# Performance work log

Hardware: AMD Instinct MI355X
Metric: run time of the kernel (lower is better)

Reference implementation:

```python
import jax, jax.numpy as jnp
import numpy as np

N_NODES = 16384
N_GRAPHS = 64
NODES_PER_GRAPH = N_NODES // N_GRAPHS
F_IN = 128
E_DIM = 256
N_HEADS = 8
MLP = 1024
N_LAYERS = 4
N_CLASSES = 10
N_EDGES = 262144
LN_EPS = 1e-5


def setup_inputs() -> dict:
    key = jax.random.key(0)
    ks = jax.random.split(key, 32)
    s = 0.02
    inp = {
        "x": jax.random.normal(ks[0], (N_NODES, F_IN), jnp.float32),
        "edge_idx": jax.random.randint(ks[1], (2, N_EDGES), 0, N_NODES, jnp.int32),
        "batch": (jnp.arange(N_NODES, dtype=jnp.int32) // NODES_PER_GRAPH),
        "pos_enc": jax.random.normal(ks[2], (N_NODES, E_DIM), jnp.float32),
        # GCNConv params (torch Linear convention: W is [out, in])
        "gcn_w": jax.random.normal(ks[3], (F_IN, F_IN), jnp.float32) * s,
        "gcn_b": jnp.zeros((F_IN,), jnp.float32),
        "cls": jax.random.normal(ks[4], (E_DIM,), jnp.float32),
        "emb_w": jax.random.normal(ks[5], (E_DIM, F_IN), jnp.float32) * s,
        "emb_b": jnp.zeros((E_DIM,), jnp.float32),
        # stacked transformer-encoder-layer params over L layers
        "in_w": jax.random.normal(ks[6], (N_LAYERS, 3 * E_DIM, E_DIM), jnp.float32) * s,
        "in_b": jnp.zeros((N_LAYERS, 3 * E_DIM), jnp.float32),
        "out_w": jax.random.normal(ks[7], (N_LAYERS, E_DIM, E_DIM), jnp.float32) * s,
        "out_b": jnp.zeros((N_LAYERS, E_DIM), jnp.float32),
        "lin1_w": jax.random.normal(ks[8], (N_LAYERS, MLP, E_DIM), jnp.float32) * s,
        "lin1_b": jnp.zeros((N_LAYERS, MLP), jnp.float32),
        "lin2_w": jax.random.normal(ks[9], (N_LAYERS, E_DIM, MLP), jnp.float32) * s,
        "lin2_b": jnp.zeros((N_LAYERS, E_DIM), jnp.float32),
        "ln1_g": jnp.ones((N_LAYERS, E_DIM), jnp.float32),
        "ln1_beta": jnp.zeros((N_LAYERS, E_DIM), jnp.float32),
        "ln2_g": jnp.ones((N_LAYERS, E_DIM), jnp.float32),
        "ln2_beta": jnp.zeros((N_LAYERS, E_DIM), jnp.float32),
        "fc_w": jax.random.normal(ks[10], (N_CLASSES, E_DIM), jnp.float32) * s,
        "fc_b": jnp.zeros((N_CLASSES,), jnp.float32),
    }
    return inp


def _layer_norm(h, g, b):
    mu = jnp.mean(h, axis=-1, keepdims=True)
    var = jnp.mean(jnp.square(h - mu), axis=-1, keepdims=True)
    return (h - mu) * jax.lax.rsqrt(var + LN_EPS) * g + b


def _gcn_conv(x, edge_idx, gcn_w, gcn_b):
    # PyG GCNConv: lin -> add self-loops -> sym-normalized scatter-add -> +bias
    xw = x @ gcn_w.T                                             # [N, F]
    ar = jnp.arange(N_NODES, dtype=edge_idx.dtype)
    ei = jnp.concatenate([edge_idx, jnp.stack([ar, ar])], axis=1)
    row, col = ei[0], ei[1]
    deg = jax.ops.segment_sum(jnp.ones(ei.shape[1], xw.dtype), col, num_segments=N_NODES)
    dinv = jax.lax.rsqrt(deg)                                    # deg >= 1 (self loops)
    norm = dinv[row] * dinv[col]                                 # [E+N]
    out = jax.ops.segment_sum(norm[:, None] * xw[row], col, num_segments=N_NODES)
    return out + gcn_b


def reference(x, edge_idx, batch, pos_enc, gcn_w, gcn_b, cls, emb_w, emb_b,
              in_w, in_b, out_w, out_b, lin1_w, lin1_b, lin2_w, lin2_b,
              ln1_g, ln1_beta, ln2_g, ln2_beta, fc_w, fc_b):
    h = _gcn_conv(x, edge_idx, gcn_w, gcn_b)
    h = jax.nn.relu(h)
    h = h @ emb_w.T + emb_b + pos_enc                            # [N, E_DIM]
    # batch = arange // NODES_PER_GRAPH (contiguous equal-size graphs):
    # per-graph loop == batched reshape
    h = h.reshape(N_GRAPHS, NODES_PER_GRAPH, E_DIM)
    cls_tok = jnp.broadcast_to(cls, (N_GRAPHS, 1, E_DIM))
    h = jnp.concatenate([cls_tok, h], axis=1)                    # [G, S, E]
    S = NODES_PER_GRAPH + 1
    dh = E_DIM // N_HEADS
    scale = 1.0 / jnp.sqrt(jnp.asarray(dh, h.dtype))
    for l in range(N_LAYERS):
        # post-LN TransformerEncoderLayer (torch default), dropout off
        qkv = jnp.einsum('gse,fe->gsf', h, in_w[l]) + in_b[l]    # [G, S, 3E]
        q, k, v = jnp.split(qkv, 3, axis=-1)
        q = q.reshape(N_GRAPHS, S, N_HEADS, dh).transpose(0, 2, 1, 3)
        k = k.reshape(N_GRAPHS, S, N_HEADS, dh).transpose(0, 2, 1, 3)
        v = v.reshape(N_GRAPHS, S, N_HEADS, dh).transpose(0, 2, 1, 3)
        att = jax.nn.softmax(jnp.einsum('ghqd,ghkd->ghqk', q, k) * scale, axis=-1)
        o = jnp.einsum('ghqk,ghkd->ghqd', att, v)
        o = o.transpose(0, 2, 1, 3).reshape(N_GRAPHS, S, E_DIM)
        o = jnp.einsum('gse,fe->gsf', o, out_w[l]) + out_b[l]
        h = _layer_norm(h + o, ln1_g[l], ln1_beta[l])
        f = jax.nn.relu(jnp.einsum('gse,me->gsm', h, lin1_w[l]) + lin1_b[l])
        f = jnp.einsum('gsm,em->gse', f, lin2_w[l]) + lin2_b[l]
        h = _layer_norm(h + f, ln2_g[l], ln2_beta[l])
    cls_out = h[:, 0, :]                                         # [G, E]
    return cls_out @ fc_w.T + fc_b                               # [G, C]
```

## Files before the change

kernel.cpp:

```cpp
#include <hip/hip_runtime.h>
#include <cstddef>

#define N_NODES 16384
#define N_GRAPHS 64
#define NPG 256
#define F_IN 128
#define E_DIM 256
#define N_HEADS 8
#define DH 32
#define MLP 1024
#define N_LAYERS 4
#define N_CLASSES 10
#define N_EDGES 262144
#define S_LEN 257
#define M_ROWS (N_GRAPHS * S_LEN)
#define M_PAD 16512
#define LN_EPS 1e-5f

typedef __attribute__((ext_vector_type(8))) short bf16x8;
typedef __attribute__((ext_vector_type(4))) float f32x4;

__device__ inline unsigned short f2b1(float f) {
    unsigned u = __float_as_uint(f);
    unsigned r = (u + 0x7fffu + ((u >> 16) & 1u)) >> 16;
    return (unsigned short)r;
}

#define GLOBAL_LOAD_LDS16(g, l) \
    __builtin_amdgcn_global_load_lds((__attribute__((address_space(1))) const void*)(g), \
                                     (__attribute__((address_space(3))) void*)(l), 16, 0, 0)

struct F2BJobs {
    const float* src[7];
    unsigned short* dst[7];
    int n4[7];
};
__global__ __launch_bounds__(256) void f2b_all(F2BJobs jobs) {
#pragma unroll 1
    for (int r = 0; r < 7; ++r) {
        const float4* s = (const float4*)jobs.src[r];
        ushort4* d = (ushort4*)jobs.dst[r];
        const int n4 = jobs.n4[r];
        for (int i = blockIdx.x * 256 + threadIdx.x; i < n4; i += gridDim.x * 256) {
            float4 v = s[i];
            ushort4 o;
            o.x = f2b1(v.x); o.y = f2b1(v.y); o.z = f2b1(v.z); o.w = f2b1(v.w);
            d[i] = o;
        }
    }
}

__global__ __launch_bounds__(256) void gemm_mfma(
    const unsigned short* __restrict__ A, const unsigned short* __restrict__ W,
    const float* __restrict__ bias, const float* __restrict__ add,
    float* __restrict__ outF, unsigned short* __restrict__ outB,
    int M, int N, int K, int relu)
{
    __shared__ __align__(16) unsigned short As0[128 * 32], As1[128 * 32];
    __shared__ __align__(16) unsigned short Bs0[128 * 32], Bs1[128 * 32];
    const int tid = threadIdx.x;
    const int wave = tid >> 6;
    const int lane = tid & 63;
    const int bm = blockIdx.y * 128;
    const int bn = blockIdx.x * 128;

    const int srow = (lane >> 2);
    const int scol = (lane & 3) * 8;
    const size_t a_r0 = (size_t)(bm + wave * 16 + srow) * K + scol;
    const size_t b_r0 = (size_t)(bn + wave * 16 + srow) * K + scol;

    const int wm = (wave & 1) * 64;
    const int wn = (wave >> 1) * 64;
    const int fr = lane & 15;
    const int fk = (lane >> 4) * 8;

    f32x4 acc[4][4];
#pragma unroll
    for (int i = 0; i < 4; ++i)
#pragma unroll
        for (int j = 0; j < 4; ++j)
            acc[i][j] = (f32x4){0.f, 0.f, 0.f, 0.f};

    auto stage = [&](unsigned short* Asb, unsigned short* Bsb, int k0) {
        GLOBAL_LOAD_LDS16(A + a_r0 + k0, Asb + wave * 512);
        GLOBAL_LOAD_LDS16(A + a_r0 + (size_t)64 * K + k0, Asb + (wave + 4) * 512);
        GLOBAL_LOAD_LDS16(W + b_r0 + k0, Bsb + wave * 512);
        GLOBAL_LOAD_LDS16(W + b_r0 + (size_t)64 * K + k0, Bsb + (wave + 4) * 512);
    };
    auto compute = [&](const unsigned short* Asb, const unsigned short* Bsb) {
        bf16x8 a[4], b[4];
#pragma unroll
        for (int i = 0; i < 4; ++i)
            a[i] = *(const bf16x8*)(Asb + (wm + i * 16 + fr) * 32 + fk);
#pragma unroll
        for (int j = 0; j < 4; ++j)
            b[j] = *(const bf16x8*)(Bsb + (wn + j * 16 + fr) * 32 + fk);
#pragma unroll
        for (int i = 0; i < 4; ++i)
#pragma unroll
            for (int j = 0; j < 4; ++j)
                acc[i][j] = __builtin_amdgcn_mfma_f32_16x16x32_bf16(a[i], b[j], acc[i][j], 0, 0, 0);
    };

    stage(As0, Bs0, 0);
    for (int k0 = 0; k0 < K; k0 += 64) {
        __syncthreads();
        if (k0 + 32 < K) stage(As1, Bs1, k0 + 32);
        compute(As0, Bs0);
        __syncthreads();
        if (k0 + 64 < K) stage(As0, Bs0, k0 + 64);
        compute(As1, Bs1);
    }

    const int er = (lane >> 4) * 4;
    const int ec = lane & 15;
#pragma unroll
    for (int j = 0; j < 4; ++j) {
        const int col = bn + wn + j * 16 + ec;
        const float bs = bias ? bias[col] : 0.f;
#pragma unroll
        for (int i = 0; i < 4; ++i) {
#pragma unroll
            for (int r = 0; r < 4; ++r) {
                const int row = bm + wm + i * 16 + er + r;
                float v = acc[i][j][r] + bs;
                if (add)  v += add[(size_t)row * N + col];
                if (relu) v = fmaxf(v, 0.f);
                if (outF) outF[(size_t)row * N + col] = v;
                if (outB) outB[(size_t)row * N + col] = f2b1(v);
            }
        }
    }
}

__global__ __launch_bounds__(256) void gemm_ln(
    const unsigned short* __restrict__ A, const unsigned short* __restrict__ W,
    const float* __restrict__ bias, const float* __restrict__ g,
    const float* __restrict__ beta,
    float* __restrict__ h, unsigned short* __restrict__ hb, int K)
{
    __shared__ __align__(16) unsigned short As0[32 * 32], As1[32 * 32];
    __shared__ __align__(16) unsigned short Bs0[256 * 32], Bs1[256 * 32];
    __shared__ float red[2][2][16][2];
    const int tid  = threadIdx.x;
    const int wave = tid >> 6;
    const int lane = tid & 63;
    const int quad = lane >> 4;
    const int l16  = lane & 15;
    const int rgrp = wave >> 1;
    const int ch   = wave & 1;
    const int bm   = blockIdx.x * 32;

    const int srow = lane >> 2;
    const int scol = (lane & 3) * 8;

    f32x4 acc[8];
#pragma unroll
    for (int j = 0; j < 8; ++j) acc[j] = (f32x4){0.f, 0.f, 0.f, 0.f};

    auto stage = [&](unsigned short* Asb, unsigned short* Bsb, int k0) {
        if (wave < 2)
            GLOBAL_LOAD_LDS16(A + (size_t)(bm + wave * 16 + srow) * K + k0 + scol,
                              Asb + wave * 512);
#pragma unroll
        for (int cc = 0; cc < 4; ++cc) {
            const int c = wave + cc * 4;
            GLOBAL_LOAD_LDS16(W + (size_t)(c * 16 + srow) * K + k0 + scol, Bsb + c * 512);
        }
    };
    auto compute = [&](const unsigned short* Asb, const unsigned short* Bsb) {
        bf16x8 a = *(const bf16x8*)(Asb + (rgrp * 16 + l16) * 32 + quad * 8);
#pragma unroll
        for (int j = 0; j < 8; ++j) {
            bf16x8 b = *(const bf16x8*)(Bsb + (ch * 128 + j * 16 + l16) * 32 + quad * 8);
            acc[j] = __builtin_amdgcn_mfma_f32_16x16x32_bf16(a, b, acc[j], 0, 0, 0);
        }
    };

    stage(As0, Bs0, 0);
    for (int k0 = 0; k0 < K; k0 += 64) {
        __syncthreads();
        if (k0 + 32 < K) stage(As1, Bs1, k0 + 32);
        compute(As0, Bs0);
        __syncthreads();
        if (k0 + 64 < K) stage(As0, Bs0, k0 + 64);
        compute(As1, Bs1);
    }

    float gv[8], bv[8], biasv[8];
#pragma unroll
    for (int j = 0; j < 8; ++j) {
        const int col = ch * 128 + j * 16 + l16;
        gv[j] = g[col]; bv[j] = beta[col]; biasv[j] = bias[col];
    }
    float v[4][8];
#pragma unroll
    for (int r = 0; r < 4; ++r) {
        const int row = bm + rgrp * 16 + quad * 4 + r;
        float s1 = 0.f, s2 = 0.f;
#pragma unroll
        for (int j = 0; j < 8; ++j) {
            const int col = ch * 128 + j * 16 + l16;
            float t = acc[j][r] + biasv[j] + h[(size_t)row * E_DIM + col];
            v[r][j] = t; s1 += t; s2 += t * t;
        }
        s1 += __shfl_xor(s1, 1, 64); s2 += __shfl_xor(s2, 1, 64);
        s1 += __shfl_xor(s1, 2, 64); s2 += __shfl_xor(s2, 2, 64);
        s1 += __shfl_xor(s1, 4, 64); s2 += __shfl_xor(s2, 4, 64);
        s1 += __shfl_xor(s1, 8, 64); s2 += __shfl_xor(s2, 8, 64);
        if (l16 == 0) { red[rgrp][ch][quad * 4 + r][0] = s1; red[rgrp][ch][quad * 4 + r][1] = s2; }
    }
    __syncthreads();
#pragma unroll
    for (int r = 0; r < 4; ++r) {
        const int row = bm + rgrp * 16 + quad * 4 + r;
        const float t1 = red[rgrp][0][quad * 4 + r][0] + red[rgrp][1][quad * 4 + r][0];
        const float t2 = red[rgrp][0][quad * 4 + r][1] + red[rgrp][1][quad * 4 + r][1];
        const float mu = t1 * (1.f / 256.f);
        const float var = t2 * (1.f / 256.f) - mu * mu;
        const float rstd = rsqrtf(var + LN_EPS);
#pragma unroll
        for (int j = 0; j < 8; ++j) {
            const int col = ch * 128 + j * 16 + l16;
            float o = (v[r][j] - mu) * rstd * gv[j] + bv[j];
            h[(size_t)row * E_DIM + col] = o;
            hb[(size_t)row * E_DIM + col] = f2b1(o);
        }
    }
}

__global__ void deg_count(const int* __restrict__ ei, float* __restrict__ deg) {
    int e = blockIdx.x * blockDim.x + threadIdx.x;
    if (e < N_EDGES) atomicAdd(&deg[ei[N_EDGES + e]], 1.0f);
}

__global__ __launch_bounds__(1024) void scan_deg(const float* __restrict__ deg,
                                                 int* __restrict__ row_start) {
    __shared__ int lds[1024];
    const int t = threadIdx.x;
    const int base = t * 16;
    int loc[16];
    int s = 0;
#pragma unroll
    for (int i = 0; i < 16; ++i) { loc[i] = s; s += (int)deg[base + i]; }
    lds[t] = s;
    __syncthreads();
    for (int off = 1; off < 1024; off <<= 1) {
        int v = lds[t];
        int u = (t >= off) ? lds[t - off] : 0;
        __syncthreads();
        lds[t] = v + u;
        __syncthreads();
    }
    const int excl = (t == 0) ? 0 : lds[t - 1];
#pragma unroll
    for (int i = 0; i < 16; ++i) row_start[base + i] = excl + loc[i];
    if (t == 1023) row_start[16384] = lds[1023];
}

__global__ void make_dinv(float* __restrict__ deg) {
    int i = blockIdx.x * blockDim.x + threadIdx.x;
    if (i < N_NODES) deg[i] = rsqrtf(deg[i] + 1.0f);
}

__global__ void scatter_edges(const int* __restrict__ ei, const float* __restrict__ dinv,
                              const int* __restrict__ row_start, int* __restrict__ cursor,
                              int* __restrict__ esrc, float* __restrict__ enrm) {
    int e = blockIdx.x * 256 + threadIdx.x;
    if (e < N_EDGES) {
        int r = ei[e], c = ei[N_EDGES + e];
        int slot = atomicAdd(&cursor[c], 1);
        int p = row_start[c] + slot;
        esrc[p] = r;
        enrm[p] = dinv[r] * dinv[c];
    }
}

__global__ __launch_bounds__(256) void gcn_gather(
    const float* __restrict__ xw, const int* __restrict__ row_start,
    const int* __restrict__ esrc, const float* __restrict__ enrm,
    const float* __restrict__ dinv, const float* __restrict__ bias,
    unsigned short* __restrict__ aggb) {
    const int n = blockIdx.x * 4 + (threadIdx.x >> 6);
    const int t = threadIdx.x & 63;
    const int e0 = row_start[n], e1 = row_start[n + 1];
    float ax = 0.f, ay = 0.f;
    for (int e = e0; e < e1; ++e) {
        int s = esrc[e];
        float w = enrm[e];
        float2 v = ((const float2*)(xw + (size_t)s * F_IN))[t];
        ax += w * v.x; ay += w * v.y;
    }
    const float di = dinv[n];
    const float w0 = di * di;
    float2 vs = ((const float2*)(xw + (size_t)n * F_IN))[t];
    ax += w0 * vs.x; ay += w0 * vs.y;
    float2 b2 = ((const float2*)bias)[t];
    ushort2 o;
    o.x = f2b1(fmaxf(ax + b2.x, 0.f));
    o.y = f2b1(fmaxf(ay + b2.y, 0.f));
    ((ushort2*)(aggb + (size_t)n * F_IN))[t] = o;
}

__global__ void assemble_h(const float* __restrict__ emb, const float* __restrict__ cls,
                           float* __restrict__ h, unsigned short* __restrict__ hb) {
    int row = blockIdx.x;
    int f = threadIdx.x;
    int g = row / S_LEN, s = row % S_LEN;
    float v = (s == 0) ? cls[f] : emb[((size_t)g * NPG + (s - 1)) * E_DIM + f];
    h[(size_t)row * E_DIM + f] = v;
    hb[(size_t)row * E_DIM + f] = f2b1(v);
}

__global__ __launch_bounds__(256) void attn_mfma(const unsigned short* __restrict__ qkvb,
                                                 unsigned short* __restrict__ ob) {
    const int g  = blockIdx.x >> 3;
    const int hh = blockIdx.x & 7;
    __shared__ __align__(16) unsigned short Ks[272 * 32];
    __shared__ __align__(16) unsigned short VT[32 * 288];
    __shared__ __align__(16) unsigned short Ps[4 * 16 * 288];
    const int tid  = threadIdx.x;
    const int wave = tid >> 6;
    const int lane = tid & 63;
    const int quad = lane >> 4;
    const int l16  = lane & 15;
    const size_t grow0 = (size_t)g * S_LEN;

    for (int s = tid; s < 272; s += 256) {
        uint4* dst = (uint4*)&Ks[s * 32];
        if (s < S_LEN) {
            const uint4* src = (const uint4*)(qkvb + (grow0 + s) * 768 + 256 + hh * 32);
            dst[0] = src[0]; dst[1] = src[1]; dst[2] = src[2]; dst[3] = src[3];
        } else {
            uint4 z = {0u, 0u, 0u, 0u};
            dst[0] = z; dst[1] = z; dst[2] = z; dst[3] = z;
        }
    }
    for (int s = tid; s < 288; s += 256) {
        unsigned short t[32];
        if (s < S_LEN) {
            const uint4* src = (const uint4*)(qkvb + (grow0 + s) * 768 + 512 + hh * 32);
            ((uint4*)t)[0] = src[0]; ((uint4*)t)[1] = src[1];
            ((uint4*)t)[2] = src[2]; ((uint4*)t)[3] = src[3];
        } else {
#pragma unroll
            for (int d = 0; d < 32; ++d) t[d] = 0;
        }
#pragma unroll
        for (int d = 0; d < 32; ++d) VT[d * 288 + s] = t[d];
    }
    unsigned short* Pw = &Ps[wave * 16 * 288];
    for (int i = lane; i < 256; i += 64)
        Pw[(i >> 4) * 288 + 272 + (i & 15)] = 0;
    __syncthreads();

    const float scale = 0.17677669529663687f;
    for (int qt = wave; qt < 17; qt += 4) {
        const int qrow_l = qt * 16 + l16;
        bf16x8 aq = *(const bf16x8*)(qkvb + (grow0 + qrow_l) * 768 + hh * 32 + quad * 8);

        f32x4 sc[17];
#pragma unroll
        for (int kt = 0; kt < 17; ++kt) {
            bf16x8 bk = *(const bf16x8*)&Ks[(kt * 16 + l16) * 32 + quad * 8];
            f32x4 z = (f32x4){0.f, 0.f, 0.f, 0.f};
            sc[kt] = __builtin_amdgcn_mfma_f32_16x16x32_bf16(aq, bk, z, 0, 0, 0);
        }

        float lsum[4] = {0.f, 0.f, 0.f, 0.f};
#pragma unroll
        for (int kt = 0; kt < 17; ++kt) {
#pragma unroll
            for (int r = 0; r < 4; ++r) {
                float p = __expf(sc[kt][r] * scale);
                if (kt == 16 && l16 != 0) p = 0.f;
                lsum[r] += p;
                Pw[(quad * 4 + r) * 288 + kt * 16 + l16] = f2b1(p);
            }
        }
#pragma unroll
        for (int r = 0; r < 4; ++r) {
            float s = lsum[r];
            s += __shfl_xor(s, 1, 64);
            s += __shfl_xor(s, 2, 64);
            s += __shfl_xor(s, 4, 64);
            s += __shfl_xor(s, 8, 64);
            lsum[r] = s;
        }

        f32x4 o0 = (f32x4){0.f, 0.f, 0.f, 0.f};
        f32x4 o1 = (f32x4){0.f, 0.f, 0.f, 0.f};
#pragma unroll
        for (int c = 0; c < 9; ++c) {
            bf16x8 ap  = *(const bf16x8*)&Pw[l16 * 288 + c * 32 + quad * 8];
            bf16x8 bv0 = *(const bf16x8*)&VT[l16 * 288 + c * 32 + quad * 8];
            bf16x8 bv1 = *(const bf16x8*)&VT[(16 + l16) * 288 + c * 32 + quad * 8];
            o0 = __builtin_amdgcn_mfma_f32_16x16x32_bf16(ap, bv0, o0, 0, 0, 0);
            o1 = __builtin_amdgcn_mfma_f32_16x16x32_bf16(ap, bv1, o1, 0, 0, 0);
        }

#pragma unroll
        for (int r = 0; r < 4; ++r) {
            int row_l = qt * 16 + quad * 4 + r;
            if (row_l < S_LEN) {
                float inv = 1.f / lsum[r];
                size_t orow = (grow0 + row_l) * E_DIM + hh * 32;
                ob[orow + l16]      = f2b1(o0[r] * inv);
                ob[orow + 16 + l16] = f2b1(o1[r] * inv);
            }
        }
    }
}

__global__ void fc_kernel(const float* __restrict__ h, const float* __restrict__ w,
                          const float* __restrict__ b, float* __restrict__ out) {
    int g = blockIdx.x;
    __shared__ float row[E_DIM];
    int t = threadIdx.x;
    row[t] = h[(size_t)g * S_LEN * E_DIM + t];
    __syncthreads();
    if (t < N_CLASSES) {
        float s = 0.f;
        for (int j = 0; j < E_DIM; ++j) s += row[j] * w[t * E_DIM + j];
        out[g * N_CLASSES + t] = s + b[t];
    }
}

extern "C" void kernel_launch(void* const* d_in, const int* in_sizes, int n_in,
                              void* d_out, int out_size, void* d_ws, size_t ws_size,
                              hipStream_t stream) {
    const float* x       = (const float*)d_in[0];
    const int*   edgei   = (const int*)  d_in[1];
    const float* pos_enc = (const float*)d_in[3];
    const float* gcn_w   = (const float*)d_in[4];
    const float* gcn_b   = (const float*)d_in[5];
    const float* cls     = (const float*)d_in[6];
    const float* emb_w   = (const float*)d_in[7];
    const float* emb_b   = (const float*)d_in[8];
    const float* in_w    = (const float*)d_in[9];
    const float* in_b    = (const float*)d_in[10];
    const float* out_w   = (const float*)d_in[11];
    const float* out_b   = (const float*)d_in[12];
    const float* lin1_w  = (const float*)d_in[13];
    const float* lin1_b  = (const float*)d_in[14];
    const float* lin2_w  = (const float*)d_in[15];
    const float* lin2_b  = (const float*)d_in[16];
    const float* ln1_g   = (const float*)d_in[17];
    const float* ln1_be  = (const float*)d_in[18];
    const float* ln2_g   = (const float*)d_in[19];
    const float* ln2_be  = (const float*)d_in[20];
    const float* fc_w    = (const float*)d_in[21];
    const float* fc_b    = (const float*)d_in[22];
    float* out = (float*)d_out;

    float* ws = (float*)d_ws;
    float* h    = ws;
    float* qkv  = h   + (size_t)M_PAD * E_DIM;
    float* xw   = qkv + (size_t)M_PAD * 768;
    float* deg  = xw  + (size_t)N_NODES * F_IN;
    int*   cursor    = (int*)(deg + N_NODES);
    int*   row_start = cursor + N_NODES;
    int*   esrc      = row_start + N_NODES + 1;
    float* enrm      = (float*)(esrc + N_EDGES);
    unsigned short* ub     = (unsigned short*)(enrm + N_EDGES);
    unsigned short* hb     = ub;
    unsigned short* attnob = hb     + (size_t)M_PAD * E_DIM;
    unsigned short* fbufb  = attnob + (size_t)M_PAD * E_DIM;
    unsigned short* xb     = fbufb  + (size_t)M_PAD * MLP;
    unsigned short* aggb   = xb     + (size_t)N_NODES * F_IN;
    unsigned short* gcn_wb = aggb   + (size_t)N_NODES * F_IN;
    unsigned short* emb_wb = gcn_wb + (size_t)F_IN * F_IN;
    unsigned short* in_wb  = emb_wb + (size_t)E_DIM * F_IN;
    unsigned short* out_wb = in_wb  + (size_t)N_LAYERS * 768 * E_DIM;
    unsigned short* lin1_wb= out_wb + (size_t)N_LAYERS * E_DIM * E_DIM;
    unsigned short* lin2_wb= lin1_wb+ (size_t)N_LAYERS * MLP * E_DIM;
    float* emb_out = qkv;
    unsigned short* qkvb = (unsigned short*)qkv;

    F2BJobs jobs;
    jobs.src[0] = x;      jobs.dst[0] = xb;      jobs.n4[0] = N_NODES * F_IN / 4;
    jobs.src[1] = gcn_w;  jobs.dst[1] = gcn_wb;  jobs.n4[1] = F_IN * F_IN / 4;
    jobs.src[2] = emb_w;  jobs.dst[2] = emb_wb;  jobs.n4[2] = E_DIM * F_IN / 4;
    jobs.src[3] = in_w;   jobs.dst[3] = in_wb;   jobs.n4[3] = N_LAYERS * 768 * E_DIM / 4;
    jobs.src[4] = out_w;  jobs.dst[4] = out_wb;  jobs.n4[4] = N_LAYERS * E_DIM * E_DIM / 4;
    jobs.src[5] = lin1_w; jobs.dst[5] = lin1_wb; jobs.n4[5] = N_LAYERS * MLP * E_DIM / 4;
    jobs.src[6] = lin2_w; jobs.dst[6] = lin2_wb; jobs.n4[6] = N_LAYERS * E_DIM * MLP / 4;
    f2b_all<<<1024, 256, 0, stream>>>(jobs);

    hipMemsetAsync(deg, 0, 2 * N_NODES * sizeof(float), stream);
    deg_count<<<(N_EDGES + 255) / 256, 256, 0, stream>>>(edgei, deg);
    scan_deg<<<1, 1024, 0, stream>>>(deg, row_start);
    make_dinv<<<(N_NODES + 255) / 256, 256, 0, stream>>>(deg);
    gemm_mfma<<<dim3(F_IN / 128, N_NODES / 128), 256, 0, stream>>>(
        xb, gcn_wb, nullptr, nullptr, xw, nullptr, N_NODES, F_IN, F_IN, 0);
    scatter_edges<<<(N_EDGES + 255) / 256, 256, 0, stream>>>(edgei, deg, row_start, cursor, esrc, enrm);
    gcn_gather<<<N_NODES / 4, 256, 0, stream>>>(xw, row_start, esrc, enrm, deg, gcn_b, aggb);

    gemm_mfma<<<dim3(E_DIM / 128, N_NODES / 128), 256, 0, stream>>>(
        aggb, emb_wb, emb_b, pos_enc, emb_out, nullptr, N_NODES, E_DIM, F_IN, 0);
    assemble_h<<<M_ROWS, E_DIM, 0, stream>>>(emb_out, cls, h, hb);

    for (int l = 0; l < N_LAYERS; ++l) {
        gemm_mfma<<<dim3(768 / 128, M_PAD / 128), 256, 0, stream>>>(
            hb, in_wb + (size_t)l * 768 * E_DIM, in_b + (size_t)l * 768, nullptr,
            nullptr, qkvb, M_PAD, 768, E_DIM, 0);
        attn_mfma<<<N_GRAPHS * N_HEADS, 256, 0, stream>>>(qkvb, attnob);
        gemm_ln<<<M_PAD / 32, 256, 0, stream>>>(
            attnob, out_wb + (size_t)l * E_DIM * E_DIM, out_b + (size_t)l * E_DIM,
            ln1_g + l * E_DIM, ln1_be + l * E_DIM, h, hb, E_DIM);
        gemm_mfma<<<dim3(MLP / 128, M_PAD / 128), 256, 0, stream>>>(
            hb, lin1_wb + (size_t)l * MLP * E_DIM, lin1_b + (size_t)l * MLP, nullptr,
            nullptr, fbufb, M_PAD, MLP, E_DIM, 1);
        gemm_ln<<<M_PAD / 32, 256, 0, stream>>>(
            fbufb, lin2_wb + (size_t)l * E_DIM * MLP, lin2_b + (size_t)l * E_DIM,
            ln2_g + l * E_DIM, ln2_be + l * E_DIM, h, hb, MLP);
    }

    fc_kernel<<<N_GRAPHS, E_DIM, 0, stream>>>(h, fc_w, fc_b, out);
}
```

Baseline: 871.0 us.

## Load GEMM+LayerNorm operands directly into registers with K-templated prefetch

The fused GEMM+LayerNorm kernel no longer stages A and W tiles through double-buffered LDS with block barriers. Each wave now loads its bf16 fragments straight from global memory into registers, keeping up to four K-steps in flight, and K becomes a template parameter so the loop fully unrolls. It also requests two blocks per CU through launch bounds. This removes LDS traffic and __syncthreads, but W rows are read by every block without LDS sharing, and register pressure rises with the prefetch depth.

```diff
diff --git a/kernel.cpp b/kernel.cpp
--- a/kernel.cpp
+++ b/kernel.cpp
@@ -133,14 +133,15 @@
     }
 }
 
-__global__ __launch_bounds__(256) void gemm_ln(
+template<int K>
+__global__ __launch_bounds__(256, 2) void gemm_ln_t(
     const unsigned short* __restrict__ A, const unsigned short* __restrict__ W,
     const float* __restrict__ bias, const float* __restrict__ g,
     const float* __restrict__ beta,
-    float* __restrict__ h, unsigned short* __restrict__ hb, int K)
+    float* __restrict__ h, unsigned short* __restrict__ hb)
 {
-    __shared__ __align__(16) unsigned short As0[32 * 32], As1[32 * 32];
-    __shared__ __align__(16) unsigned short Bs0[256 * 32], Bs1[256 * 32];
+    constexpr int NSTEP = K / 32;
+    constexpr int RD = (NSTEP < 4) ? NSTEP : 4;
     __shared__ float red[2][2][16][2];
     const int tid  = threadIdx.x;
     const int wave = tid >> 6;
@@ -151,40 +152,38 @@
     const int ch   = wave & 1;
     const int bm   = blockIdx.x * 32;
 
-    const int srow = lane >> 2;
-    const int scol = (lane & 3) * 8;
+    const unsigned short* Ap = A + (size_t)(bm + rgrp * 16 + l16) * K + quad * 8;
+    const unsigned short* Bp[8];
+#pragma unroll
+    for (int j = 0; j < 8; ++j)
+        Bp[j] = W + (size_t)(ch * 128 + j * 16 + l16) * K + quad * 8;
 
     f32x4 acc[8];
 #pragma unroll
     for (int j = 0; j < 8; ++j) acc[j] = (f32x4){0.f, 0.f, 0.f, 0.f};
 
-    auto stage = [&](unsigned short* Asb, unsigned short* Bsb, int k0) {
-        if (wave < 2)
-            GLOBAL_LOAD_LDS16(A + (size_t)(bm + wave * 16 + srow) * K + k0 + scol,
-                              Asb + wave * 512);
-#pragma unroll
-        for (int cc = 0; cc < 4; ++cc) {
-            const int c = wave + cc * 4;
-            GLOBAL_LOAD_LDS16(W + (size_t)(c * 16 + srow) * K + k0 + scol, Bsb + c * 512);
-        }
-    };
-    auto compute = [&](const unsigned short* Asb, const unsigned short* Bsb) {
-        bf16x8 a = *(const bf16x8*)(Asb + (rgrp * 16 + l16) * 32 + quad * 8);
-#pragma unroll
-        for (int j = 0; j < 8; ++j) {
-            bf16x8 b = *(const bf16x8*)(Bsb + (ch * 128 + j * 16 + l16) * 32 + quad * 8);
-            acc[j] = __builtin_amdgcn_mfma_f32_16x16x32_bf16(a, b, acc[j], 0, 0, 0);
-        }
-    };
-
-    stage(As0, Bs0, 0);
-    for (int k0 = 0; k0 < K; k0 += 64) {
-        __syncthreads();
-        if (k0 + 32 < K) stage(As1, Bs1, k0 + 32);
-        compute(As0, Bs0);
-        __syncthreads();
-        if (k0 + 64 < K) stage(As0, Bs0, k0 + 64);
-        compute(As1, Bs1);
+    bf16x8 areg[RD];
+    bf16x8 breg[RD][8];
+#pragma unroll
+    for (int p = 0; p < RD; ++p) {
+        areg[p] = *(const bf16x8*)(Ap + p * 32);
+#pragma unroll
+        for (int j = 0; j < 8; ++j)
+            breg[p][j] = *(const bf16x8*)(Bp[j] + p * 32);
+    }
+
+#pragma unroll
+    for (int s = 0; s < NSTEP; ++s) {
+        const int sl = s % RD;
+#pragma unroll
+        for (int j = 0; j < 8; ++j)
+            acc[j] = __builtin_amdgcn_mfma_f32_16x16x32_bf16(areg[sl], breg[sl][j], acc[j], 0, 0, 0);
+        if (s + RD < NSTEP) {
+            areg[sl] = *(const bf16x8*)(Ap + (s + RD) * 32);
+#pragma unroll
+            for (int j = 0; j < 8; ++j)
+                breg[sl][j] = *(const bf16x8*)(Bp[j] + (s + RD) * 32);
+        }
     }
 
     float gv[8], bv[8], biasv[8];
@@ -505,15 +504,15 @@
             hb, in_wb + (size_t)l * 768 * E_DIM, in_b + (size_t)l * 768, nullptr,
             nullptr, qkvb, M_PAD, 768, E_DIM, 0);
         attn_mfma<<<N_GRAPHS * N_HEADS, 256, 0, stream>>>(qkvb, attnob);
-        gemm_ln<<<M_PAD / 32, 256, 0, stream>>>(
+        gemm_ln_t<E_DIM><<<M_PAD / 32, 256, 0, stream>>>(
             attnob, out_wb + (size_t)l * E_DIM * E_DIM, out_b + (size_t)l * E_DIM,
-            ln1_g + l * E_DIM, ln1_be + l * E_DIM, h, hb, E_DIM);
+            ln1_g + l * E_DIM, ln1_be + l * E_DIM, h, hb);
         gemm_mfma<<<dim3(MLP / 128, M_PAD / 128), 256, 0, stream>>>(
             hb, lin1_wb + (size_t)l * MLP * E_DIM, lin1_b + (size_t)l * MLP, nullptr,
             nullptr, fbufb, M_PAD, MLP, E_DIM, 1);
-        gemm_ln<<<M_PAD / 32, 256, 0, stream>>>(
-            fbufb, lin2_wb + (size_t)l * E_DIM * MLP, lin2_b + (size_t)l * E_DIM,
-            ln2_g + l * E_DIM, ln2_be + l * E_DIM, h, hb, MLP);
+        gemm_ln_t<MLP><<<M_PAD / 32, 256, 0, stream>>>(
+            fbufb, lin2_wb + (size_t)l * MLP * E_DIM, lin2_b + (size_t)l * E_DIM,
+            ln2_g + l * E_DIM, ln2_be + l * E_DIM, h, hb);
     }
 
     fc_kernel<<<N_GRAPHS, E_DIM, 0, stream>>>(h, fc_w, fc_b, out);
```

Result: slower. 1.148 ms (+31.9%).

## Unfuse GEMM+LayerNorm into generic 128x128 GEMM plus separate LN kernel

Applied to the files above, without the earlier changes.

Replaces the fused gemm_ln kernel, which used 32-row tiles covering the full 256-wide output, with the generic 128x128 gemm_mfma writing the residual sum to an fp32 temp buffer. A new per-row ln_apply kernel then normalizes and writes h and its bf16 copy. The aim is the better data reuse of the larger GEMM tile. The cost is extra kernel launches and an fp32 round trip of the temp buffer through memory.

```diff
diff --git a/kernel.cpp b/kernel.cpp
--- a/kernel.cpp
+++ b/kernel.cpp
@@ -133,100 +133,38 @@
     }
 }
 
-__global__ __launch_bounds__(256) void gemm_ln(
-    const unsigned short* __restrict__ A, const unsigned short* __restrict__ W,
-    const float* __restrict__ bias, const float* __restrict__ g,
-    const float* __restrict__ beta,
-    float* __restrict__ h, unsigned short* __restrict__ hb, int K)
-{
-    __shared__ __align__(16) unsigned short As0[32 * 32], As1[32 * 32];
-    __shared__ __align__(16) unsigned short Bs0[256 * 32], Bs1[256 * 32];
-    __shared__ float red[2][2][16][2];
-    const int tid  = threadIdx.x;
-    const int wave = tid >> 6;
-    const int lane = tid & 63;
-    const int quad = lane >> 4;
-    const int l16  = lane & 15;
-    const int rgrp = wave >> 1;
-    const int ch   = wave & 1;
-    const int bm   = blockIdx.x * 32;
-
-    const int srow = lane >> 2;
-    const int scol = (lane & 3) * 8;
-
-    f32x4 acc[8];
-#pragma unroll
-    for (int j = 0; j < 8; ++j) acc[j] = (f32x4){0.f, 0.f, 0.f, 0.f};
-
-    auto stage = [&](unsigned short* Asb, unsigned short* Bsb, int k0) {
-        if (wave < 2)
-            GLOBAL_LOAD_LDS16(A + (size_t)(bm + wave * 16 + srow) * K + k0 + scol,
-                              Asb + wave * 512);
-#pragma unroll
-        for (int cc = 0; cc < 4; ++cc) {
-            const int c = wave + cc * 4;
-            GLOBAL_LOAD_LDS16(W + (size_t)(c * 16 + srow) * K + k0 + scol, Bsb + c * 512);
-        }
-    };
-    auto compute = [&](const unsigned short* Asb, const unsigned short* Bsb) {
-        bf16x8 a = *(const bf16x8*)(Asb + (rgrp * 16 + l16) * 32 + quad * 8);
-#pragma unroll
-        for (int j = 0; j < 8; ++j) {
-            bf16x8 b = *(const bf16x8*)(Bsb + (ch * 128 + j * 16 + l16) * 32 + quad * 8);
-            acc[j] = __builtin_amdgcn_mfma_f32_16x16x32_bf16(a, b, acc[j], 0, 0, 0);
-        }
-    };
-
-    stage(As0, Bs0, 0);
-    for (int k0 = 0; k0 < K; k0 += 64) {
-        __syncthreads();
-        if (k0 + 32 < K) stage(As1, Bs1, k0 + 32);
-        compute(As0, Bs0);
-        __syncthreads();
-        if (k0 + 64 < K) stage(As0, Bs0, k0 + 64);
-        compute(As1, Bs1);
-    }
-
-    float gv[8], bv[8], biasv[8];
-#pragma unroll
-    for (int j = 0; j < 8; ++j) {
-        const int col = ch * 128 + j * 16 + l16;
-        gv[j] = g[col]; bv[j] = beta[col]; biasv[j] = bias[col];
-    }
-    float v[4][8];
-#pragma unroll
-    for (int r = 0; r < 4; ++r) {
-        const int row = bm + rgrp * 16 + quad * 4 + r;
-        float s1 = 0.f, s2 = 0.f;
-#pragma unroll
-        for (int j = 0; j < 8; ++j) {
-            const int col = ch * 128 + j * 16 + l16;
-            float t = acc[j][r] + biasv[j] + h[(size_t)row * E_DIM + col];
-            v[r][j] = t; s1 += t; s2 += t * t;
-        }
-        s1 += __shfl_xor(s1, 1, 64); s2 += __shfl_xor(s2, 1, 64);
-        s1 += __shfl_xor(s1, 2, 64); s2 += __shfl_xor(s2, 2, 64);
-        s1 += __shfl_xor(s1, 4, 64); s2 += __shfl_xor(s2, 4, 64);
-        s1 += __shfl_xor(s1, 8, 64); s2 += __shfl_xor(s2, 8, 64);
-        if (l16 == 0) { red[rgrp][ch][quad * 4 + r][0] = s1; red[rgrp][ch][quad * 4 + r][1] = s2; }
-    }
+__global__ __launch_bounds__(256) void ln_apply(const float* __restrict__ tmp,
+                                                const float* __restrict__ g,
+                                                const float* __restrict__ b,
+                                                float* __restrict__ h,
+                                                unsigned short* __restrict__ hb) {
+    __shared__ float ws1[4], ws2[4];
+    __shared__ float mu_s, rstd_s;
+    const int row = blockIdx.x;
+    const int t = threadIdx.x;
+    size_t idx = (size_t)row * E_DIM + t;
+    float v = tmp[idx];
+    float s1 = v, s2 = v * v;
+#pragma unroll
+    for (int off = 32; off > 0; off >>= 1) {
+        s1 += __shfl_down(s1, off, 64);
+        s2 += __shfl_down(s2, off, 64);
+    }
+    int wid = t >> 6, lane = t & 63;
+    if (lane == 0) { ws1[wid] = s1; ws2[wid] = s2; }
     __syncthreads();
-#pragma unroll
-    for (int r = 0; r < 4; ++r) {
-        const int row = bm + rgrp * 16 + quad * 4 + r;
-        const float t1 = red[rgrp][0][quad * 4 + r][0] + red[rgrp][1][quad * 4 + r][0];
-        const float t2 = red[rgrp][0][quad * 4 + r][1] + red[rgrp][1][quad * 4 + r][1];
-        const float mu = t1 * (1.f / 256.f);
-        const float var = t2 * (1.f / 256.f) - mu * mu;
-        const float rstd = rsqrtf(var + LN_EPS);
-#pragma unroll
-        for (int j = 0; j < 8; ++j) {
-            const int col = ch * 128 + j * 16 + l16;
-            float o = (v[r][j] - mu) * rstd * gv[j] + bv[j];
-            h[(size_t)row * E_DIM + col] = o;
-            hb[(size_t)row * E_DIM + col] = f2b1(o);
-        }
-    }
+    if (t == 0) {
+        float a1 = ws1[0] + ws1[1] + ws1[2] + ws1[3];
+        float a2 = ws2[0] + ws2[1] + ws2[2] + ws2[3];
+        float mu = a1 * (1.f / 256.f);
+        float var = a2 * (1.f / 256.f) - mu * mu;
+        mu_s = mu;
+        rstd_s = rsqrtf(var + LN_EPS);
+    }
+    __syncthreads();
+    float o = (v - mu_s) * rstd_s * g[t] + b[t];
+    h[idx] = o;
+    hb[idx] = f2b1(o);
 }
 
 __global__ void deg_count(const int* __restrict__ ei, float* __restrict__ deg) {
@@ -455,7 +393,8 @@
 
     float* ws = (float*)d_ws;
     float* h    = ws;
-    float* qkv  = h   + (size_t)M_PAD * E_DIM;
+    float* tmp  = h   + (size_t)M_PAD * E_DIM;
+    float* qkv  = tmp + (size_t)M_PAD * E_DIM;
     float* xw   = qkv + (size_t)M_PAD * 768;
     float* deg  = xw  + (size_t)N_NODES * F_IN;
     int*   cursor    = (int*)(deg + N_NODES);
@@ -505,15 +444,17 @@
             hb, in_wb + (size_t)l * 768 * E_DIM, in_b + (size_t)l * 768, nullptr,
             nullptr, qkvb, M_PAD, 768, E_DIM, 0);
         attn_mfma<<<N_GRAPHS * N_HEADS, 256, 0, stream>>>(qkvb, attnob);
-        gemm_ln<<<M_PAD / 32, 256, 0, stream>>>(
-            attnob, out_wb + (size_t)l * E_DIM * E_DIM, out_b + (size_t)l * E_DIM,
-            ln1_g + l * E_DIM, ln1_be + l * E_DIM, h, hb, E_DIM);
+        gemm_mfma<<<dim3(E_DIM / 128, M_PAD / 128), 256, 0, stream>>>(
+            attnob, out_wb + (size_t)l * E_DIM * E_DIM, out_b + (size_t)l * E_DIM, h,
+            tmp, nullptr, M_PAD, E_DIM, E_DIM, 0);
+        ln_apply<<<M_ROWS, E_DIM, 0, stream>>>(tmp, ln1_g + l * E_DIM, ln1_be + l * E_DIM, h, hb);
         gemm_mfma<<<dim3(MLP / 128, M_PAD / 128), 256, 0, stream>>>(
             hb, lin1_wb + (size_t)l * MLP * E_DIM, lin1_b + (size_t)l * MLP, nullptr,
             nullptr, fbufb, M_PAD, MLP, E_DIM, 1);
-        gemm_ln<<<M_PAD / 32, 256, 0, stream>>>(
-            fbufb, lin2_wb + (size_t)l * E_DIM * MLP, lin2_b + (size_t)l * E_DIM,
-            ln2_g + l * E_DIM, ln2_be + l * E_DIM, h, hb, MLP);
+        gemm_mfma<<<dim3(E_DIM / 128, M_PAD / 128), 256, 0, stream>>>(
+            fbufb, lin2_wb + (size_t)l * MLP * E_DIM, lin2_b + (size_t)l * E_DIM, h,
+            tmp, nullptr, M_PAD, E_DIM, MLP, 0);
+        ln_apply<<<M_ROWS, E_DIM, 0, stream>>>(tmp, ln2_g + l * E_DIM, ln2_be + l * E_DIM, h, hb);
     }
 
     fc_kernel<<<N_GRAPHS, E_DIM, 0, stream>>>(h, fc_w, fc_b, out);
```

Result: slower. 1.046 ms (+20.0%).
